# Kernel tuning notes

Measured on AMD Instinct MI355X. Metric: run time of the kernel, lower is better.

Reference implementation:

```python
import math
import jax, jax.numpy as jnp
import numpy as np

B, S, D, H = 2, 2048, 1024, 16
DK = D // H


def setup_inputs() -> dict:
    key = jax.random.key(0)
    ks = jax.random.split(key, 12)
    scale = 1.0 / math.sqrt(D)
    inp = {
        "q": jax.random.normal(ks[0], (B, S, D), jnp.float32),
        "k": jax.random.normal(ks[1], (B, S, D), jnp.float32),
        "v": jax.random.normal(ks[2], (B, S, D), jnp.float32),
        # causal mask, broadcast over batch and heads (mask==0 -> -inf)
        "mask": jnp.tril(jnp.ones((S, S), jnp.int32))[None, None, :, :],
        "Wq": jax.random.normal(ks[3], (D, D), jnp.float32) * scale,
        "bq": jnp.zeros((D,), jnp.float32),
        "Wk": jax.random.normal(ks[4], (D, D), jnp.float32) * scale,
        "bk": jnp.zeros((D,), jnp.float32),
        "Wv": jax.random.normal(ks[5], (D, D), jnp.float32) * scale,
        "bv": jnp.zeros((D,), jnp.float32),
        "Wo": jax.random.normal(ks[6], (D, D), jnp.float32) * scale,
        "bo": jnp.zeros((D,), jnp.float32),
    }
    return inp


def reference(q, k, v, mask, Wq, bq, Wk, bk, Wv, bv, Wo, bo):
    def proj(x, W, b):
        # [B,S,D] -> [B,H,S,DK]
        return (x @ W + b).reshape(B, -1, H, DK).transpose(0, 2, 1, 3)

    Q = proj(q, Wq, bq)
    K = proj(k, Wk, bk)
    V = proj(v, Wv, bv)
    scores = jnp.einsum("bhqd,bhkd->bhqk", Q, K) / math.sqrt(DK)  # [B,H,S,S]
    scores = jnp.where(mask == 0, -jnp.inf, scores)
    attn = jax.nn.softmax(scores, axis=-1)  # dropout p=0.0 -> identity
    ctx = jnp.einsum("bhqk,bhkd->bhqd", attn, V)
    ctx = ctx.transpose(0, 2, 1, 3).reshape(B, -1, D)  # [B,S,D]
    return ctx @ Wo + bo
```

## Files before the change

### kernel.cpp

```cpp
#include <hip/hip_runtime.h>
#include <stdint.h>

#define BB 2
#define SS 2048
#define DD 1024
#define HH 16
#define DK 64

#define QSCALE 0.1803368801111204f
#define NEGS -1.0e30f

typedef short s16x8 __attribute__((ext_vector_type(8)));
typedef float f32x4 __attribute__((ext_vector_type(4)));
typedef unsigned short u16x4 __attribute__((ext_vector_type(4)));
typedef unsigned int u32x4 __attribute__((ext_vector_type(4)));

static __device__ __forceinline__ unsigned short f2bf(float f) {
  unsigned int u = __builtin_bit_cast(unsigned int, f);
  u = (u + 0x7fffu + ((u >> 16) & 1u)) >> 16;
  return (unsigned short)u;
}

static __device__ __forceinline__ float bf2f(unsigned short s) {
  unsigned int u = ((unsigned int)s) << 16;
  return __builtin_bit_cast(float, u);
}

static __device__ __forceinline__ unsigned int cvtpk(float lo, float hi) {
  unsigned int r;
  asm("v_cvt_pk_bf16_f32 %0, %1, %2" : "=v"(r) : "v"(lo), "v"(hi));
  return r;
}

static __device__ __forceinline__ f32x4 mfma16(s16x8 a, s16x8 b, f32x4 c) {
  return __builtin_amdgcn_mfma_f32_16x16x32_bf16(a, b, c, 0, 0, 0);
}

static __device__ __forceinline__ void gload_lds16(const void* g, void* l) {
  __builtin_amdgcn_global_load_lds(
      (const __attribute__((address_space(1))) unsigned int*)g,
      (__attribute__((address_space(3))) unsigned int*)l, 16, 0, 0);
}

__global__ __launch_bounds__(256) void cvt3_kernel(const float* __restrict__ q,
                                                   const float* __restrict__ k,
                                                   const float* __restrict__ v,
                                                   unsigned short* __restrict__ qb,
                                                   unsigned short* __restrict__ kb,
                                                   unsigned short* __restrict__ vb) {
  int sel = blockIdx.y;
  const float* in = (sel == 0) ? q : ((sel == 1) ? k : v);
  unsigned short* out = (sel == 0) ? qb : ((sel == 1) ? kb : vb);
  int i = blockIdx.x * 256 + threadIdx.x;
  f32x4 vv = ((const f32x4*)in)[i];
  u16x4 o;
  o.x = f2bf(vv.x); o.y = f2bf(vv.y); o.z = f2bf(vv.z); o.w = f2bf(vv.w);
  ((u16x4*)out)[i] = o;
}

__global__ __launch_bounds__(256) void transpose_w4_kernel(const float* __restrict__ Wq,
                                                           const float* __restrict__ Wk,
                                                           const float* __restrict__ Wv,
                                                           const float* __restrict__ Wo,
                                                           unsigned short* __restrict__ WTbase) {
  __shared__ float t[32][33];
  int z = blockIdx.z;
  const float* W = (z == 0) ? Wq : ((z == 1) ? Wk : ((z == 2) ? Wv : Wo));
  float scale = (z == 0) ? QSCALE : 1.0f;
  unsigned short* WT = WTbase + (size_t)z * DD * DD;
  int n0 = blockIdx.x * 32, k0 = blockIdx.y * 32;
  int tx = threadIdx.x, ty = threadIdx.y;
  for (int i = 0; i < 4; ++i)
    t[ty + 8 * i][tx] = W[(size_t)(k0 + ty + 8 * i) * DD + n0 + tx];
  __syncthreads();
  for (int i = 0; i < 4; ++i)
    WT[(size_t)(n0 + ty + 8 * i) * DD + k0 + tx] = f2bf(t[tx][ty + 8 * i] * scale);
}

__global__ __launch_bounds__(256) void gemm_qkv_kernel(
    const unsigned short* __restrict__ qb, const unsigned short* __restrict__ kb,
    const unsigned short* __restrict__ vb, const unsigned short* __restrict__ WTbase,
    const float* __restrict__ bq, const float* __restrict__ bk,
    const float* __restrict__ bv, unsigned short* __restrict__ Qh,
    unsigned short* __restrict__ Kh, unsigned short* __restrict__ VhT) {
  const int K = DD;
  __shared__ __align__(16) unsigned short Alds[2][128 * 64];
  __shared__ __align__(16) unsigned short Blds[2][64 * 64];
  int tid = threadIdx.x;
  int lane = tid & 63, wave = tid >> 6;
  int g = lane >> 4, r16 = lane & 15;

  int bid = blockIdx.x;
  int logical = (bid & 7) * 192 + (bid >> 3);
  int y = logical >> 4, xn = logical & 15;
  int seg = y >> 5;
  int m0 = (y & 31) * 128, n0 = xn * 64;
  int wm = (wave >> 1) * 64, wn = (wave & 1) * 32;

  const unsigned short* A = (seg == 0) ? qb : ((seg == 1) ? kb : vb);
  const unsigned short* BT = WTbase + (size_t)seg * DD * DD;
  const float* bias = (seg == 0) ? bq : ((seg == 1) ? bk : bv);
  float bsc = (seg == 0) ? QSCALE : 1.0f;

  f32x4 acc[4][2] = {};

  int ar[4], ac[4];
#pragma unroll
  for (int i = 0; i < 4; ++i) {
    int c = tid + 256 * i;
    ar[i] = c >> 3;
    ac[i] = (c & 7) ^ (ar[i] & 7);
  }
  int br[2], bc[2];
#pragma unroll
  for (int i = 0; i < 2; ++i) {
    int c = tid + 256 * i;
    br[i] = c >> 3;
    bc[i] = (c & 7) ^ (br[i] & 7);
  }

#define STAGE_AB(buf, k0)                                                          \
  do {                                                                             \
    _Pragma("unroll") for (int i = 0; i < 4; ++i)                                  \
        gload_lds16((const char*)(A + (size_t)(m0 + ar[i]) * K + (k0)) + ac[i] * 16, \
                    (char*)Alds[buf] + wave * 1024 + i * 4096);                    \
    _Pragma("unroll") for (int i = 0; i < 2; ++i)                                  \
        gload_lds16((const char*)(BT + (size_t)(n0 + br[i]) * K + (k0)) + bc[i] * 16, \
                    (char*)Blds[buf] + wave * 1024 + i * 4096);                    \
  } while (0)

  STAGE_AB(0, 0);
  int cur = 0;

  for (int k0 = 0; k0 < K; k0 += 64) {
    __syncthreads();
    if (k0 + 64 < K) STAGE_AB(cur ^ 1, k0 + 64);

#pragma unroll
    for (int ks = 0; ks < 2; ++ks) {
      s16x8 af[4], bfr[2];
#pragma unroll
      for (int mt = 0; mt < 4; ++mt) {
        int row = wm + mt * 16 + r16;
        int ch = (ks * 4 + g) ^ (row & 7);
        af[mt] = *(const s16x8*)((const char*)Alds[cur] + row * 128 + ch * 16);
      }
#pragma unroll
      for (int nt = 0; nt < 2; ++nt) {
        int row = wn + nt * 16 + r16;
        int ch = (ks * 4 + g) ^ (row & 7);
        bfr[nt] = *(const s16x8*)((const char*)Blds[cur] + row * 128 + ch * 16);
      }
      __builtin_amdgcn_s_setprio(1);
#pragma unroll
      for (int mt = 0; mt < 4; ++mt)
#pragma unroll
        for (int nt = 0; nt < 2; ++nt)
          acc[mt][nt] = mfma16(af[mt], bfr[nt], acc[mt][nt]);
      __builtin_amdgcn_s_setprio(0);
    }
    cur ^= 1;
  }
#undef STAGE_AB

  unsigned short* outh = (seg == 0) ? Qh : Kh;
#pragma unroll
  for (int nt = 0; nt < 2; ++nt) {
    int col = n0 + wn + nt * 16 + r16;
    int h = col >> 6, dk = col & (DK - 1);
    float bvv = bias[col] * bsc;
#pragma unroll
    for (int mt = 0; mt < 4; ++mt) {
      int row0g = m0 + wm + mt * 16 + g * 4;
      int bb = row0g >> 11, s0 = row0g & (SS - 1);
      if (seg == 2) {
        u16x4 o;
#pragma unroll
        for (int rr = 0; rr < 4; ++rr) o[rr] = f2bf(acc[mt][nt][rr] + bvv);
        *(u16x4*)&VhT[((size_t)(bb * HH + h) * DK + dk) * SS + s0] = o;
      } else {
#pragma unroll
        for (int rr = 0; rr < 4; ++rr) {
          outh[(((size_t)bb * HH + h) * SS + s0 + rr) * DK + dk] =
              f2bf(acc[mt][nt][rr] + bvv);
        }
      }
    }
  }
}

__global__ __launch_bounds__(256) void gemm_out_kernel(const unsigned short* __restrict__ A,
                                                       const unsigned short* __restrict__ BT,
                                                       const float* __restrict__ bias,
                                                       float* __restrict__ out) {
  const int K = DD;
  __shared__ __align__(16) unsigned short Alds[2][128 * 32];
  __shared__ __align__(16) unsigned short Blds[2][64 * 32];
  int tid = threadIdx.x;
  int lane = tid & 63, wave = tid >> 6;
  int g = lane >> 4, r16 = lane & 15;

  int bid = blockIdx.x;
  int logical = (bid & 7) * 64 + (bid >> 3);
  int m0 = (logical >> 4) * 128, n0 = (logical & 15) * 64;
  int wm = (wave >> 1) * 64, wn = (wave & 1) * 32;

  f32x4 acc[4][2] = {};

  int c0 = tid, c1 = tid + 256;
  int arow0 = c0 >> 2, arow1 = c1 >> 2;
  int as0 = (c0 & 3) ^ ((arow0 >> 1) & 3);
  int as1 = (c1 & 3) ^ ((arow1 >> 1) & 3);

#define STAGE_AB(buf, k0)                                                        \
  do {                                                                           \
    gload_lds16((const char*)(A + (size_t)(m0 + arow0) * K + (k0)) + as0 * 16,   \
                (char*)Alds[buf] + wave * 1024);                                 \
    gload_lds16((const char*)(A + (size_t)(m0 + arow1) * K + (k0)) + as1 * 16,   \
                (char*)Alds[buf] + wave * 1024 + 4096);                          \
    gload_lds16((const char*)(BT + (size_t)(n0 + arow0) * K + (k0)) + as0 * 16,  \
                (char*)Blds[buf] + wave * 1024);                                 \
  } while (0)

  STAGE_AB(0, 0);
  int cur = 0;

  for (int k0 = 0; k0 < K; k0 += 32) {
    __syncthreads();
    if (k0 + 32 < K) STAGE_AB(cur ^ 1, k0 + 32);

    s16x8 af[4], bfr[2];
#pragma unroll
    for (int mt = 0; mt < 4; ++mt) {
      int row = wm + mt * 16 + r16;
      int ch = g ^ ((row >> 1) & 3);
      af[mt] = *(const s16x8*)((const char*)Alds[cur] + row * 64 + ch * 16);
    }
#pragma unroll
    for (int nt = 0; nt < 2; ++nt) {
      int row = wn + nt * 16 + r16;
      int ch = g ^ ((row >> 1) & 3);
      bfr[nt] = *(const s16x8*)((const char*)Blds[cur] + row * 64 + ch * 16);
    }
    __builtin_amdgcn_s_setprio(1);
#pragma unroll
    for (int mt = 0; mt < 4; ++mt)
#pragma unroll
      for (int nt = 0; nt < 2; ++nt)
        acc[mt][nt] = mfma16(af[mt], bfr[nt], acc[mt][nt]);
    __builtin_amdgcn_s_setprio(0);
    cur ^= 1;
  }
#undef STAGE_AB

#pragma unroll
  for (int nt = 0; nt < 2; ++nt) {
    int col = n0 + wn + nt * 16 + r16;
    float bvv = bias[col];
#pragma unroll
    for (int mt = 0; mt < 4; ++mt) {
#pragma unroll
      for (int rr = 0; rr < 4; ++rr) {
        int rowg = m0 + wm + mt * 16 + g * 4 + rr;
        out[(size_t)rowg * DD + col] = acc[mt][nt][rr] + bvv;
      }
    }
  }
}

__global__ __launch_bounds__(256) void attn_kernel(const unsigned short* __restrict__ Qh,
                                                   const unsigned short* __restrict__ Kh,
                                                   const unsigned short* __restrict__ VhT,
                                                   unsigned short* __restrict__ ctx,
                                                   unsigned short* __restrict__ Opart,
                                                   float2* __restrict__ mlpart) {
  __shared__ __align__(16) unsigned short Klds[2][64 * 64];
  __shared__ __align__(16) unsigned short Vlds[2][64 * 64];

  int tid = threadIdx.x;
  int lane = tid & 63, wave = tid >> 6;
  int g = lane >> 4, r16 = lane & 15;
  int bid = blockIdx.x;
  int x = bid >> 3;
  int pid = x & 7;
  int hf = (x >> 3) & 1;
  int bh = ((x >> 4) << 3) | (bid & 7);

  int tilesA = hf ? 0 : 2 * pid + 2;
  const int NT = 17;
  int q0A = pid * 128, q0B = (15 - pid) * 128;
  int kvoffB = hf ? (15 - 2 * pid) : 0;

  const unsigned short* Qb = Qh + (size_t)bh * SS * DK;
  const char* Kb = (const char*)(Kh + (size_t)bh * SS * DK);
  const char* Vb = (const char*)(VhT + (size_t)bh * DK * SS);

  int a_ = r16 >> 2, b_ = r16 & 3;
  int rbase = 8 * a_ + b_;
  int sk = b_ + 4 * (a_ & 1);

  int c0 = tid, c1 = tid + 256;
  int row0 = c0 >> 3, row1 = c1 >> 3;
  int skst0 = ((row0 & 3) | (((row0 >> 3) & 1) << 2));
  int skst1 = ((row1 & 3) | (((row1 >> 3) & 1) << 2));
  int kc0 = (c0 & 7) ^ skst0, kc1 = (c1 & 7) ^ skst1;
  int vc0 = (c0 & 7) ^ (row0 & 7), vc1 = (c1 & 7) ^ (row1 & 7);

#define KV_OF(t) ((hf ? (kvoffB + (t)) : (((t) < tilesA) ? (t) : ((t) - tilesA))) * 64)
#define STAGE_KV(buf, kv0)                                                   \
  do {                                                                       \
    gload_lds16(Kb + ((size_t)((kv0) + row0) * 128) + kc0 * 16,              \
                (char*)Klds[buf] + wave * 1024);                             \
    gload_lds16(Kb + ((size_t)((kv0) + row1) * 128) + kc1 * 16,              \
                (char*)Klds[buf] + wave * 1024 + 4096);                      \
    gload_lds16(Vb + ((size_t)row0 * SS + (kv0)) * 2 + vc0 * 16,             \
                (char*)Vlds[buf] + wave * 1024);                             \
    gload_lds16(Vb + ((size_t)row1 * SS + (kv0)) * 2 + vc1 * 16,             \
                (char*)Vlds[buf] + wave * 1024 + 4096);                      \
  } while (0)

  int b = bh >> 4, h = bh & (HH - 1);

  int qw0 = (hf ? q0B : q0A) + wave * 32;
  s16x8 aq[2][2];
#pragma unroll
  for (int mt = 0; mt < 2; ++mt)
#pragma unroll
    for (int kc = 0; kc < 2; ++kc)
      aq[mt][kc] = *(const s16x8*)(Qb + (size_t)(qw0 + mt * 16 + r16) * DK + kc * 32 + g * 8);

  STAGE_KV(0, KV_OF(0));

  f32x4 accd[2][4] = {};
  float mrow[2] = {-INFINITY, -INFINITY};
  float lrow[2] = {0.0f, 0.0f};

  for (int t = 0; t < NT; ++t) {
    if (hf == 0 && t == tilesA) {
#pragma unroll
      for (int mt = 0; mt < 2; ++mt) {
        float inv = 1.0f / lrow[mt];
        int srow = qw0 + mt * 16 + r16;
#pragma unroll
        for (int dsub = 0; dsub < 4; ++dsub) {
          int d0 = dsub * 16 + 4 * g;
          u16x4 o;
#pragma unroll
          for (int rr = 0; rr < 4; ++rr) o[rr] = f2bf(accd[mt][dsub][rr] * inv);
          *(u16x4*)&ctx[(((size_t)b * SS + srow) * HH + h) * DK + d0] = o;
        }
      }
      qw0 = q0B + wave * 32;
#pragma unroll
      for (int mt = 0; mt < 2; ++mt)
#pragma unroll
        for (int kc = 0; kc < 2; ++kc)
          aq[mt][kc] = *(const s16x8*)(Qb + (size_t)(qw0 + mt * 16 + r16) * DK + kc * 32 + g * 8);
#pragma unroll
      for (int mt = 0; mt < 2; ++mt) {
#pragma unroll
        for (int dsub = 0; dsub < 4; ++dsub) accd[mt][dsub] = (f32x4){0.f, 0.f, 0.f, 0.f};
        mrow[mt] = -INFINITY;
        lrow[mt] = 0.0f;
      }
    }

    int kv0 = KV_OF(t);

    __syncthreads();
    if (t + 1 < NT) STAGE_KV((t + 1) & 1, KV_OF(t + 1));

    const char* Kc = (const char*)Klds[t & 1];
    const char* Vc = (const char*)Vlds[t & 1];

    f32x4 sf[2][4] = {};
    __builtin_amdgcn_s_setprio(1);
#pragma unroll
    for (int kc = 0; kc < 2; ++kc) {
      s16x8 bk[4];
#pragma unroll
      for (int nt = 0; nt < 4; ++nt) {
        int row = rbase + 4 * (nt & 1) + 32 * (nt >> 1);
        int ch = (kc * 4 + g) ^ sk;
        bk[nt] = *(const s16x8*)(Kc + row * 128 + ch * 16);
      }
#pragma unroll
      for (int nt = 0; nt < 4; ++nt) {
        sf[0][nt] = mfma16(bk[nt], aq[0][kc], sf[0][nt]);
        sf[1][nt] = mfma16(bk[nt], aq[1][kc], sf[1][nt]);
      }
    }
    __builtin_amdgcn_s_setprio(0);

    s16x8 av[2][4];
#pragma unroll
    for (int c = 0; c < 2; ++c)
#pragma unroll
      for (int dsub = 0; dsub < 4; ++dsub) {
        int row = dsub * 16 + r16;
        int ch = (c * 4 + g) ^ (row & 7);
        av[c][dsub] = *(const s16x8*)(Vc + row * 128 + ch * 16);
      }

    bool domask = (kv0 + 63 > qw0);
    unsigned int pk[2][2][4];
#pragma unroll
    for (int mt = 0; mt < 2; ++mt) {
      if (domask) {
        int thr = qw0 + mt * 16 + r16 - kv0 - 8 * g;
#pragma unroll
        for (int nt = 0; nt < 4; ++nt) {
          int koff = 4 * (nt & 1) + 32 * (nt >> 1);
#pragma unroll
          for (int rr = 0; rr < 4; ++rr)
            if (koff + rr > thr) sf[mt][nt][rr] = NEGS;
        }
      }

      float m0v = fmaxf(fmaxf(sf[mt][0][0], sf[mt][0][1]), fmaxf(sf[mt][0][2], sf[mt][0][3]));
      float m1v = fmaxf(fmaxf(sf[mt][1][0], sf[mt][1][1]), fmaxf(sf[mt][1][2], sf[mt][1][3]));
      float m2v = fmaxf(fmaxf(sf[mt][2][0], sf[mt][2][1]), fmaxf(sf[mt][2][2], sf[mt][2][3]));
      float m3v = fmaxf(fmaxf(sf[mt][3][0], sf[mt][3][1]), fmaxf(sf[mt][3][2], sf[mt][3][3]));
      float tmax = fmaxf(fmaxf(m0v, m1v), fmaxf(m2v, m3v));
      tmax = fmaxf(tmax, __shfl_xor(tmax, 16));
      tmax = fmaxf(tmax, __shfl_xor(tmax, 32));

      if (!__all(tmax <= mrow[mt])) {
        float mn = fmaxf(mrow[mt], tmax);
        float fc = __builtin_amdgcn_exp2f(mrow[mt] - mn);
        lrow[mt] *= fc;
        mrow[mt] = mn;
#pragma unroll
        for (int dsub = 0; dsub < 4; ++dsub)
#pragma unroll
          for (int rr = 0; rr < 4; ++rr) accd[mt][dsub][rr] *= fc;
      }

      float pf[4][4];
#pragma unroll
      for (int nt = 0; nt < 4; ++nt)
#pragma unroll
        for (int rr = 0; rr < 4; ++rr)
          pf[nt][rr] = __builtin_amdgcn_exp2f(sf[mt][nt][rr] - mrow[mt]);
      float s0v = (pf[0][0] + pf[0][1]) + (pf[0][2] + pf[0][3]);
      float s1v = (pf[1][0] + pf[1][1]) + (pf[1][2] + pf[1][3]);
      float s2v = (pf[2][0] + pf[2][1]) + (pf[2][2] + pf[2][3]);
      float s3v = (pf[3][0] + pf[3][1]) + (pf[3][2] + pf[3][3]);
      float su = (s0v + s1v) + (s2v + s3v);
      su += __shfl_xor(su, 16);
      su += __shfl_xor(su, 32);
      lrow[mt] += su;

#pragma unroll
      for (int c = 0; c < 2; ++c) {
        pk[mt][c][0] = cvtpk(pf[2 * c][0], pf[2 * c][1]);
        pk[mt][c][1] = cvtpk(pf[2 * c][2], pf[2 * c][3]);
        pk[mt][c][2] = cvtpk(pf[2 * c + 1][0], pf[2 * c + 1][1]);
        pk[mt][c][3] = cvtpk(pf[2 * c + 1][2], pf[2 * c + 1][3]);
      }
    }

    __builtin_amdgcn_s_setprio(1);
#pragma unroll
    for (int c = 0; c < 2; ++c) {
      s16x8 pb0 = __builtin_bit_cast(s16x8, *(u32x4*)pk[0][c]);
      s16x8 pb1 = __builtin_bit_cast(s16x8, *(u32x4*)pk[1][c]);
#pragma unroll
      for (int dsub = 0; dsub < 4; ++dsub) {
        accd[0][dsub] = mfma16(av[c][dsub], pb0, accd[0][dsub]);
        accd[1][dsub] = mfma16(av[c][dsub], pb1, accd[1][dsub]);
      }
    }
    __builtin_amdgcn_s_setprio(0);
  }

#pragma unroll
  for (int mt = 0; mt < 2; ++mt) {
    size_t prow = ((size_t)bh * 8 + pid) * 128 + wave * 32 + mt * 16 + r16;
    float inv = 1.0f / lrow[mt];
    unsigned short* Op = Opart + ((size_t)hf * 32768 + prow) * 64;
#pragma unroll
    for (int dsub = 0; dsub < 4; ++dsub) {
      int d0 = dsub * 16 + 4 * g;
      u16x4 o;
#pragma unroll
      for (int rr = 0; rr < 4; ++rr) o[rr] = f2bf(accd[mt][dsub][rr] * inv);
      *(u16x4*)&Op[d0] = o;
    }
    if (g == 0) mlpart[(size_t)hf * 32768 + prow] = make_float2(mrow[mt], lrow[mt]);
  }
#undef STAGE_KV
#undef KV_OF
}

__global__ __launch_bounds__(256) void combine_kernel(const unsigned short* __restrict__ Opart,
                                                      const float2* __restrict__ mlpart,
                                                      unsigned short* __restrict__ ctx) {
  int idx = blockIdx.x * 256 + threadIdx.x;
  int row = idx >> 4;
  int d0 = (idx & 15) * 4;
  float2 ml0 = mlpart[row];
  float2 ml1 = mlpart[32768 + row];
  float m = fmaxf(ml0.x, ml1.x);
  float w0 = __builtin_amdgcn_exp2f(ml0.x - m) * ml0.y;
  float w1 = __builtin_amdgcn_exp2f(ml1.x - m) * ml1.y;
  float inv = 1.0f / (w0 + w1);
  w0 *= inv;
  w1 *= inv;
  u16x4 a = *(const u16x4*)(Opart + (size_t)row * 64 + d0);
  u16x4 bb4 = *(const u16x4*)(Opart + ((size_t)32768 + row) * 64 + d0);
  u16x4 o;
#pragma unroll
  for (int j = 0; j < 4; ++j) o[j] = f2bf(bf2f(a[j]) * w0 + bf2f(bb4[j]) * w1);
  int p = row >> 7, rin = row & 127;
  int bh = p >> 3, pid = p & 7;
  int srow = (15 - pid) * 128 + rin;
  int b = bh >> 4, h = bh & (HH - 1);
  *(u16x4*)&ctx[(((size_t)b * SS + srow) * HH + h) * DK + d0] = o;
}

extern "C" void kernel_launch(void* const* d_in, const int* in_sizes, int n_in,
                              void* d_out, int out_size, void* d_ws, size_t ws_size,
                              hipStream_t stream) {
  const float* q = (const float*)d_in[0];
  const float* k = (const float*)d_in[1];
  const float* v = (const float*)d_in[2];
  const float* Wq = (const float*)d_in[4];
  const float* bq = (const float*)d_in[5];
  const float* Wk = (const float*)d_in[6];
  const float* bk = (const float*)d_in[7];
  const float* Wv = (const float*)d_in[8];
  const float* bv = (const float*)d_in[9];
  const float* Wo = (const float*)d_in[10];
  const float* bo = (const float*)d_in[11];

  char* ws = (char*)d_ws;
  const size_t MB = 1ull << 20;
  unsigned short* qb = (unsigned short*)(ws + 0 * MB);
  unsigned short* kb = (unsigned short*)(ws + 8 * MB);
  unsigned short* vb = (unsigned short*)(ws + 16 * MB);
  unsigned short* WTbase = (unsigned short*)(ws + 24 * MB);
  unsigned short* WoT = (unsigned short*)(ws + 30 * MB);
  unsigned short* Qh = (unsigned short*)(ws + 32 * MB);
  unsigned short* Kh = (unsigned short*)(ws + 40 * MB);
  unsigned short* VhT = (unsigned short*)(ws + 48 * MB);
  unsigned short* ctx = (unsigned short*)(ws + 0 * MB);
  unsigned short* Opart = (unsigned short*)(ws + 8 * MB);
  float2* mlpart = (float2*)(ws + 24 * MB);

  const int n4 = BB * SS * DD / 4;

  cvt3_kernel<<<dim3(n4 / 256, 3), 256, 0, stream>>>(q, k, v, qb, kb, vb);

  dim3 tb(32, 8);
  transpose_w4_kernel<<<dim3(32, 32, 4), tb, 0, stream>>>(Wq, Wk, Wv, Wo, WTbase);

  gemm_qkv_kernel<<<1536, 256, 0, stream>>>(qb, kb, vb, WTbase,
                                            bq, bk, bv, Qh, Kh, VhT);

  attn_kernel<<<512, 256, 0, stream>>>(Qh, Kh, VhT, ctx, Opart, mlpart);

  combine_kernel<<<2048, 256, 0, stream>>>(Opart, mlpart, ctx);

  gemm_out_kernel<<<512, 256, 0, stream>>>(ctx, WoT, bo, (float*)d_out);
}
```

Before: 120.8 us.

## Read K and V tiles directly from global memory instead of LDS staging

Removes the double-buffered LDS staging of K/V tiles, the async global-to-LDS copies and the per-tile __syncthreads. Each wave now loads its MFMA operands for K and transposed V straight from global memory, relying on L1/L2 caching for reuse across the four waves. This drops the barrier and LDS traffic, but every wave fetches the same K/V data redundantly and there is no prefetch overlap, so the loop may stall on global memory latency.

After: 144.9 us. 1.2x slower.

```diff
diff --git a/kernel.cpp b/kernel.cpp
--- a/kernel.cpp
+++ b/kernel.cpp
@@ -274,9 +274,6 @@
                                                    unsigned short* __restrict__ ctx,
                                                    unsigned short* __restrict__ Opart,
                                                    float2* __restrict__ mlpart) {
-  __shared__ __align__(16) unsigned short Klds[2][64 * 64];
-  __shared__ __align__(16) unsigned short Vlds[2][64 * 64];
-
   int tid = threadIdx.x;
   int lane = tid & 63, wave = tid >> 6;
   int g = lane >> 4, r16 = lane & 15;
@@ -292,32 +289,13 @@
   int kvoffB = hf ? (15 - 2 * pid) : 0;
 
   const unsigned short* Qb = Qh + (size_t)bh * SS * DK;
-  const char* Kb = (const char*)(Kh + (size_t)bh * SS * DK);
-  const char* Vb = (const char*)(VhT + (size_t)bh * DK * SS);
+  const unsigned short* Kb = Kh + (size_t)bh * SS * DK;
+  const unsigned short* Vb = VhT + (size_t)bh * DK * SS;
 
   int a_ = r16 >> 2, b_ = r16 & 3;
   int rbase = 8 * a_ + b_;
-  int sk = b_ + 4 * (a_ & 1);
-
-  int c0 = tid, c1 = tid + 256;
-  int row0 = c0 >> 3, row1 = c1 >> 3;
-  int skst0 = ((row0 & 3) | (((row0 >> 3) & 1) << 2));
-  int skst1 = ((row1 & 3) | (((row1 >> 3) & 1) << 2));
-  int kc0 = (c0 & 7) ^ skst0, kc1 = (c1 & 7) ^ skst1;
-  int vc0 = (c0 & 7) ^ (row0 & 7), vc1 = (c1 & 7) ^ (row1 & 7);
 
 #define KV_OF(t) ((hf ? (kvoffB + (t)) : (((t) < tilesA) ? (t) : ((t) - tilesA))) * 64)
-#define STAGE_KV(buf, kv0)                                                   \
-  do {                                                                       \
-    gload_lds16(Kb + ((size_t)((kv0) + row0) * 128) + kc0 * 16,              \
-                (char*)Klds[buf] + wave * 1024);                             \
-    gload_lds16(Kb + ((size_t)((kv0) + row1) * 128) + kc1 * 16,              \
-                (char*)Klds[buf] + wave * 1024 + 4096);                      \
-    gload_lds16(Vb + ((size_t)row0 * SS + (kv0)) * 2 + vc0 * 16,             \
-                (char*)Vlds[buf] + wave * 1024);                             \
-    gload_lds16(Vb + ((size_t)row1 * SS + (kv0)) * 2 + vc1 * 16,             \
-                (char*)Vlds[buf] + wave * 1024 + 4096);                      \
-  } while (0)
 
   int b = bh >> 4, h = bh & (HH - 1);
 
@@ -328,8 +306,6 @@
 #pragma unroll
     for (int kc = 0; kc < 2; ++kc)
       aq[mt][kc] = *(const s16x8*)(Qb + (size_t)(qw0 + mt * 16 + r16) * DK + kc * 32 + g * 8);
-
-  STAGE_KV(0, KV_OF(0));
 
   f32x4 accd[2][4] = {};
   float mrow[2] = {-INFINITY, -INFINITY};
@@ -367,39 +343,31 @@
 
     int kv0 = KV_OF(t);
 
-    __syncthreads();
-    if (t + 1 < NT) STAGE_KV((t + 1) & 1, KV_OF(t + 1));
-
-    const char* Kc = (const char*)Klds[t & 1];
-    const char* Vc = (const char*)Vlds[t & 1];
-
     f32x4 sf[2][4] = {};
-    __builtin_amdgcn_s_setprio(1);
 #pragma unroll
     for (int kc = 0; kc < 2; ++kc) {
       s16x8 bk[4];
 #pragma unroll
       for (int nt = 0; nt < 4; ++nt) {
-        int row = rbase + 4 * (nt & 1) + 32 * (nt >> 1);
-        int ch = (kc * 4 + g) ^ sk;
-        bk[nt] = *(const s16x8*)(Kc + row * 128 + ch * 16);
-      }
+        int row = kv0 + rbase + 4 * (nt & 1) + 32 * (nt >> 1);
+        bk[nt] = *(const s16x8*)(Kb + (size_t)row * DK + kc * 32 + g * 8);
+      }
+      __builtin_amdgcn_s_setprio(1);
 #pragma unroll
       for (int nt = 0; nt < 4; ++nt) {
         sf[0][nt] = mfma16(bk[nt], aq[0][kc], sf[0][nt]);
         sf[1][nt] = mfma16(bk[nt], aq[1][kc], sf[1][nt]);
       }
-    }
-    __builtin_amdgcn_s_setprio(0);
+      __builtin_amdgcn_s_setprio(0);
+    }
 
     s16x8 av[2][4];
 #pragma unroll
     for (int c = 0; c < 2; ++c)
 #pragma unroll
       for (int dsub = 0; dsub < 4; ++dsub) {
-        int row = dsub * 16 + r16;
-        int ch = (c * 4 + g) ^ (row & 7);
-        av[c][dsub] = *(const s16x8*)(Vc + row * 128 + ch * 16);
+        int d = dsub * 16 + r16;
+        av[c][dsub] = *(const s16x8*)(Vb + (size_t)d * SS + kv0 + c * 32 + g * 8);
       }
 
     bool domask = (kv0 + 63 > qw0);
@@ -489,7 +457,6 @@
     }
     if (g == 0) mlpart[(size_t)hf * 32768 + prow] = make_float2(mrow[mt], lrow[mt]);
   }
-#undef STAGE_KV
 #undef KV_OF
 }
 
```

## Defer PV MFMAs by one KV tile to overlap with next softmax

Applied to the files above, without the earlier changes.

The P·V matrix multiplies for a KV tile are now held back and issued in the next iteration, right after that tile's QK MFMAs. The V fragments and packed P values are kept in registers across iterations, and pending work is flushed at the query-block switch and after the loop. The aim is to let the exp and reduction VALU work of softmax interleave with the matrix-core work instead of running serially. In exchange, the extra live registers (V fragments plus packed P) may reduce occupancy or cause spills.

After: 120.5 us. No clear change (-0.3%).

```diff
diff --git a/kernel.cpp b/kernel.cpp
--- a/kernel.cpp
+++ b/kernel.cpp
@@ -319,6 +319,20 @@
                 (char*)Vlds[buf] + wave * 1024 + 4096);                      \
   } while (0)
 
+#define DO_PV()                                                              \
+  do {                                                                       \
+    __builtin_amdgcn_s_setprio(1);                                           \
+    _Pragma("unroll") for (int c = 0; c < 2; ++c) {                          \
+      s16x8 pb0 = __builtin_bit_cast(s16x8, *(u32x4*)spk[0][c]);             \
+      s16x8 pb1 = __builtin_bit_cast(s16x8, *(u32x4*)spk[1][c]);             \
+      _Pragma("unroll") for (int dsub = 0; dsub < 4; ++dsub) {               \
+        accd[0][dsub] = mfma16(sav[c][dsub], pb0, accd[0][dsub]);            \
+        accd[1][dsub] = mfma16(sav[c][dsub], pb1, accd[1][dsub]);            \
+      }                                                                      \
+    }                                                                        \
+    __builtin_amdgcn_s_setprio(0);                                           \
+  } while (0)
+
   int b = bh >> 4, h = bh & (HH - 1);
 
   int qw0 = (hf ? q0B : q0A) + wave * 32;
@@ -335,8 +349,13 @@
   float mrow[2] = {-INFINITY, -INFINITY};
   float lrow[2] = {0.0f, 0.0f};
 
+  s16x8 sav[2][4];
+  unsigned int spk[2][2][4];
+  bool pend = false;
+
   for (int t = 0; t < NT; ++t) {
     if (hf == 0 && t == tilesA) {
+      if (pend) { DO_PV(); pend = false; }
 #pragma unroll
       for (int mt = 0; mt < 2; ++mt) {
         float inv = 1.0f / lrow[mt];
@@ -392,18 +411,18 @@
     }
     __builtin_amdgcn_s_setprio(0);
 
-    s16x8 av[2][4];
+    if (pend) DO_PV();
+
 #pragma unroll
     for (int c = 0; c < 2; ++c)
 #pragma unroll
       for (int dsub = 0; dsub < 4; ++dsub) {
         int row = dsub * 16 + r16;
         int ch = (c * 4 + g) ^ (row & 7);
-        av[c][dsub] = *(const s16x8*)(Vc + row * 128 + ch * 16);
+        sav[c][dsub] = *(const s16x8*)(Vc + row * 128 + ch * 16);
       }
 
     bool domask = (kv0 + 63 > qw0);
-    unsigned int pk[2][2][4];
 #pragma unroll
     for (int mt = 0; mt < 2; ++mt) {
       if (domask) {
@@ -453,26 +472,17 @@
 
 #pragma unroll
       for (int c = 0; c < 2; ++c) {
-        pk[mt][c][0] = cvtpk(pf[2 * c][0], pf[2 * c][1]);
-        pk[mt][c][1] = cvtpk(pf[2 * c][2], pf[2 * c][3]);
-        pk[mt][c][2] = cvtpk(pf[2 * c + 1][0], pf[2 * c + 1][1]);
-        pk[mt][c][3] = cvtpk(pf[2 * c + 1][2], pf[2 * c + 1][3]);
-      }
-    }
-
-    __builtin_amdgcn_s_setprio(1);
-#pragma unroll
-    for (int c = 0; c < 2; ++c) {
-      s16x8 pb0 = __builtin_bit_cast(s16x8, *(u32x4*)pk[0][c]);
-      s16x8 pb1 = __builtin_bit_cast(s16x8, *(u32x4*)pk[1][c]);
-#pragma unroll
-      for (int dsub = 0; dsub < 4; ++dsub) {
-        accd[0][dsub] = mfma16(av[c][dsub], pb0, accd[0][dsub]);
-        accd[1][dsub] = mfma16(av[c][dsub], pb1, accd[1][dsub]);
-      }
-    }
-    __builtin_amdgcn_s_setprio(0);
-  }
+        spk[mt][c][0] = cvtpk(pf[2 * c][0], pf[2 * c][1]);
+        spk[mt][c][1] = cvtpk(pf[2 * c][2], pf[2 * c][3]);
+        spk[mt][c][2] = cvtpk(pf[2 * c + 1][0], pf[2 * c + 1][1]);
+        spk[mt][c][3] = cvtpk(pf[2 * c + 1][2], pf[2 * c + 1][3]);
+      }
+    }
+
+    pend = true;
+  }
+
+  if (pend) DO_PV();
 
 #pragma unroll
   for (int mt = 0; mt < 2; ++mt) {
@@ -491,6 +501,7 @@
   }
 #undef STAGE_KV
 #undef KV_OF
+#undef DO_PV
 }
 
 __global__ __launch_bounds__(256) void combine_kernel(const unsigned short* __restrict__ Opart,
```
